# Optimization experiments

Hardware: AMD Instinct MI355X
Metric: run time of the kernel (lower is better)

Reference implementation:

```python
import jax, jax.numpy as jnp
import numpy as np

N_NODES = 100000


def gcn_conv(x, src, dst, W, b, n):
    # x: [N, F_in]; src/dst: [E+N] (self-loops already appended)
    h = x @ W  # [N, F_out]
    deg = jax.ops.segment_sum(jnp.ones_like(dst, dtype=h.dtype), dst, num_segments=n)
    dinv = jnp.where(deg > 0, jax.lax.rsqrt(deg), 0.0)
    norm = dinv[src] * dinv[dst]  # [E+N]
    msgs = h[src] * norm[:, None]  # gather + scale
    out = jax.ops.segment_sum(msgs, dst, num_segments=n)  # scatter-add at dst
    return out + b


def setup_inputs() -> dict:
    key = jax.random.key(0)
    k1, k2, k3, ke = jax.random.split(key, 4)
    d = 64
    x = jax.random.normal(k1, (N_NODES, d), dtype=jnp.float32)
    edge_index = jax.random.randint(ke, (2, 1000000), 0, N_NODES, dtype=jnp.int64)
    s = 1.0 / np.sqrt(d)
    W1 = jax.random.normal(k2, (d, d), dtype=jnp.float32) * s
    b1 = jnp.zeros((d,), dtype=jnp.float32)
    W2 = jax.random.normal(k3, (d, d), dtype=jnp.float32) * s
    b2 = jnp.zeros((d,), dtype=jnp.float32)
    return {"x": x, "edge_index": edge_index, "W1": W1, "b1": b1, "W2": W2, "b2": b2}


def reference(x, edge_index, W1, b1, W2, b2):
    n = x.shape[0]
    loops = jnp.arange(n, dtype=edge_index.dtype)
    src = jnp.concatenate([edge_index[0], loops])
    dst = jnp.concatenate([edge_index[1], loops])
    h = gcn_conv(x, src, dst, W1, b1, n)
    h = jax.nn.relu(h)
    out = gcn_conv(h, src, dst, W2, b2, n)
    return out
```

## Files before the change

kernel.cpp:

```cpp
#include <hip/hip_runtime.h>

#define F 64
#define NCH 256

typedef __attribute__((ext_vector_type(8))) short bf16x8;
typedef __attribute__((ext_vector_type(4))) float f32x4;

static __device__ __forceinline__ unsigned short f2bf(float f) {
    unsigned u = __float_as_uint(f);
    return (unsigned short)((u + 0x7fffu + ((u >> 16) & 1u)) >> 16);
}
static __device__ __forceinline__ float bflo(unsigned u) { return __uint_as_float(u << 16); }
static __device__ __forceinline__ float bfhi(unsigned u) { return __uint_as_float(u & 0xffff0000u); }

__global__ __launch_bounds__(256) void k_histprep(const int* __restrict__ dst,
                                                  int* __restrict__ histM,
                                                  const float* __restrict__ W1,
                                                  const float* __restrict__ W2,
                                                  unsigned short* __restrict__ W1t,
                                                  unsigned short* __restrict__ W2t,
                                                  int E, int chunk, int NB) {
    const int t = threadIdx.x;
    if (blockIdx.x >= NCH) {
        int which = blockIdx.x - NCH;
        const float* W = which ? W2 : W1;
        unsigned short* Wt = which ? W2t : W1t;
#pragma unroll
        for (int i = 0; i < 16; ++i) {
            int e = t + i * 256;
            int n = e >> 6, k = e & 63;
            Wt[e] = f2bf(W[k * 64 + n]);
        }
        return;
    }
    extern __shared__ int h[];
    for (int i = t; i < NB; i += 256) h[i] = 0;
    __syncthreads();
    const int lo = blockIdx.x * chunk;
    const int hi = min(E, lo + chunk);
    for (int e = lo + t; e < hi; e += 256) {
        atomicAdd(&h[dst[e] >> 8], 1);
    }
    __syncthreads();
    for (int i = t; i < NB; i += 256) histM[i * NCH + blockIdx.x] = h[i];
}

__global__ __launch_bounds__(256) void s_part(const int* __restrict__ v,
                                              int* __restrict__ part, int M) {
    __shared__ int sd[256];
    const int t = threadIdx.x;
    const int base = blockIdx.x * 1024 + t * 4;
    int s = 0;
    if (base + 3 < M) {
        int4 d = *(const int4*)&v[base];
        s = d.x + d.y + d.z + d.w;
    } else {
#pragma unroll
        for (int j = 0; j < 4; ++j) if (base + j < M) s += v[base + j];
    }
    sd[t] = s;
    __syncthreads();
    for (int off = 128; off > 0; off >>= 1) {
        if (t < off) sd[t] += sd[t + off];
        __syncthreads();
    }
    if (t == 0) part[blockIdx.x] = sd[0];
}

__global__ __launch_bounds__(256) void s_scanp(int* __restrict__ part, int nb) {
    __shared__ int sums[256];
    const int t = threadIdx.x;
    int s = (t < nb) ? part[t] : 0;
    sums[t] = s;
    __syncthreads();
    for (int off = 1; off < 256; off <<= 1) {
        int v = (t >= off) ? sums[t - off] : 0;
        __syncthreads();
        sums[t] += v;
        __syncthreads();
    }
    if (t < nb) part[t] = sums[t] - s;
}

__global__ __launch_bounds__(256) void s_emit(int* __restrict__ v,
                                              const int* __restrict__ part, int M) {
    __shared__ int sums[256];
    const int t = threadIdx.x;
    const int base = blockIdx.x * 1024 + t * 4;
    int d0 = 0, d1 = 0, d2 = 0, d3 = 0;
    if (base + 3 < M) {
        int4 d = *(const int4*)&v[base];
        d0 = d.x; d1 = d.y; d2 = d.z; d3 = d.w;
    } else {
        if (base + 0 < M) d0 = v[base + 0];
        if (base + 1 < M) d1 = v[base + 1];
        if (base + 2 < M) d2 = v[base + 2];
        if (base + 3 < M) d3 = v[base + 3];
    }
    int tot = d0 + d1 + d2 + d3;
    sums[t] = tot;
    __syncthreads();
    for (int off = 1; off < 256; off <<= 1) {
        int x = (t >= off) ? sums[t - off] : 0;
        __syncthreads();
        sums[t] += x;
        __syncthreads();
    }
    int o0 = part[blockIdx.x] + sums[t] - tot;
    int e0 = o0, e1 = o0 + d0, e2 = e1 + d1, e3 = e2 + d2;
    if (base + 3 < M) {
        *(int4*)&v[base] = make_int4(e0, e1, e2, e3);
    } else {
        int ee[4] = {e0, e1, e2, e3};
        for (int j = 0; j < 4; ++j) if (base + j < M) v[base + j] = ee[j];
    }
}

__global__ __launch_bounds__(256) void k_scatter2(const int* __restrict__ src,
                                                  const int* __restrict__ dst,
                                                  const int* __restrict__ scanM,
                                                  int* __restrict__ ebuf,
                                                  int E, int chunk, int NB) {
    extern __shared__ int cur[];
    const int t = threadIdx.x;
    for (int i = t; i < NB; i += 256) cur[i] = scanM[i * NCH + blockIdx.x];
    __syncthreads();
    const int lo = blockIdx.x * chunk;
    const int hi = min(E, lo + chunk);
    for (int e = lo + t; e < hi; e += 256) {
        int s = src[e];
        int d = dst[e];
        int p = atomicAdd(&cur[d >> 8], 1);
        ebuf[p] = s | ((d & 255) << 17);
    }
}

__global__ __launch_bounds__(256) void k_csr(const int* __restrict__ ebuf,
                                             const int* __restrict__ scanM,
                                             int* __restrict__ rowptr,
                                             int* __restrict__ csr,
                                             float* __restrict__ dinv,
                                             int N, int E, int NB) {
    __shared__ int hist[256];
    __shared__ int scn[256];
    __shared__ int cur[256];
    const int t = threadIdx.x;
    const int bkt = blockIdx.x;
    const int beg = scanM[bkt * NCH];
    const int end = (bkt + 1 < NB) ? scanM[(bkt + 1) * NCH] : E;

    hist[t] = 0;
    __syncthreads();
    for (int e = beg + t; e < end; e += 256)
        atomicAdd(&hist[((unsigned)ebuf[e]) >> 17], 1);
    __syncthreads();

    scn[t] = hist[t];
    __syncthreads();
    for (int off = 1; off < 256; off <<= 1) {
        int v = (t >= off) ? scn[t - off] : 0;
        __syncthreads();
        scn[t] += v;
        __syncthreads();
    }

    {
        int excl = scn[t] - hist[t];
        int rp = beg + excl;
        int node = (bkt << 8) + t;
        cur[t] = rp;
        if (node < N) {
            rowptr[node] = rp;
            dinv[node] = rsqrtf((float)(hist[t] + 1));
        }
    }
    if (bkt == NB - 1 && t == 0) rowptr[N] = E;
    __syncthreads();

    for (int e = beg + t; e < end; e += 256) {
        int pk = ebuf[e];
        int p = atomicAdd(&cur[((unsigned)pk) >> 17], 1);
        csr[p] = pk & 0x1FFFF;
    }
}

__global__ __launch_bounds__(256) void k_gemm1(const float* __restrict__ X,
                                               const unsigned short* __restrict__ W1t,
                                               const float* __restrict__ dinv,
                                               unsigned short* __restrict__ hs, int N) {
    __shared__ unsigned short Wl[64 * 72];
    __shared__ unsigned short Xs[64 * 72];
    const int t = threadIdx.x;
    const int row0 = blockIdx.x * 64;

#pragma unroll
    for (int i = 0; i < 2; ++i) {
        int idx = t + i * 256;
        int n = idx >> 3, k = (idx & 7) * 8;
        *(uint4*)&Wl[n * 72 + k] = ((const uint4*)W1t)[idx];
    }
#pragma unroll
    for (int i = 0; i < 4; ++i) {
        int idx = t + i * 256;
        int r = idx >> 4, c = (idx & 15) * 4;
        int gr = row0 + r;
        float4 v = make_float4(0.f, 0.f, 0.f, 0.f);
        if (gr < N) v = *(const float4*)&X[(size_t)gr * F + c];
        unsigned p0 = (unsigned)f2bf(v.x) | ((unsigned)f2bf(v.y) << 16);
        unsigned p1 = (unsigned)f2bf(v.z) | ((unsigned)f2bf(v.w) << 16);
        *(uint2*)&Xs[r * 72 + c] = make_uint2(p0, p1);
    }
    __syncthreads();

    const int w    = t >> 6;
    const int lane = t & 63;
    const int l15  = lane & 15;
    const int quad = lane >> 4;

    bf16x8 bf[4][2];
#pragma unroll
    for (int ct = 0; ct < 4; ++ct)
#pragma unroll
        for (int kc = 0; kc < 2; ++kc)
            bf[ct][kc] = *(const bf16x8*)&Wl[(ct * 16 + l15) * 72 + kc * 32 + quad * 8];

    const int am = w * 16 + l15;
    bf16x8 af0 = *(const bf16x8*)&Xs[am * 72 + quad * 8];
    bf16x8 af1 = *(const bf16x8*)&Xs[am * 72 + 32 + quad * 8];

    f32x4 acc[4];
#pragma unroll
    for (int ct = 0; ct < 4; ++ct) {
        f32x4 z = {0.f, 0.f, 0.f, 0.f};
        z = __builtin_amdgcn_mfma_f32_16x16x32_bf16(af0, bf[ct][0], z, 0, 0, 0);
        z = __builtin_amdgcn_mfma_f32_16x16x32_bf16(af1, bf[ct][1], z, 0, 0, 0);
        acc[ct] = z;
    }

    float dv[4];
#pragma unroll
    for (int r = 0; r < 4; ++r) {
        int row = row0 + w * 16 + quad * 4 + r;
        dv[r] = (row < N) ? dinv[row] : 0.f;
    }
#pragma unroll
    for (int ct = 0; ct < 4; ++ct) {
#pragma unroll
        for (int r = 0; r < 4; ++r) {
            int row = row0 + w * 16 + quad * 4 + r;
            if (row < N)
                hs[(size_t)row * F + ct * 16 + l15] = f2bf(acc[ct][r] * dv[r]);
        }
    }
}

__global__ __launch_bounds__(512) void k_aggmm(const unsigned short* __restrict__ hs1,
                                               const int* __restrict__ rowptr,
                                               const int* __restrict__ csr,
                                               const unsigned short* __restrict__ W2t,
                                               const float* __restrict__ b1,
                                               unsigned short* __restrict__ hs2, int N) {
    __shared__ unsigned short Act[256 * 72];
    __shared__ unsigned short Wl[64 * 72];
    __shared__ float sdv[256];
    const int t = threadIdx.x;
    const int node0 = blockIdx.x << 8;

    {
        int idx = t;
        int n = idx >> 3, k = (idx & 7) * 8;
        *(uint4*)&Wl[n * 72 + k] = ((const uint4*)W2t)[idx];
    }

    const int lane = t & 7;
    const int nsub = t >> 3;
    const uint4* hsb = (const uint4*)hs1;
    float4 bb0 = *(const float4*)&b1[lane * 8];
    float4 bb1 = *(const float4*)&b1[lane * 8 + 4];

#pragma unroll
    for (int it = 0; it < 4; ++it) {
        int local = it * 64 + nsub;
        int node = node0 + local;
        float sc = 0.f;
        unsigned p0 = 0, p1 = 0, p2 = 0, p3 = 0;
        if (node < N) {
            int beg = rowptr[node];
            int end = rowptr[node + 1];
            sc = rsqrtf((float)(end - beg + 1));
            float a0, a1, a2, a3, a4, a5, a6, a7;
            {
                uint4 u = hsb[(size_t)node * 8 + lane];
                a0 = bflo(u.x); a1 = bfhi(u.x);
                a2 = bflo(u.y); a3 = bfhi(u.y);
                a4 = bflo(u.z); a5 = bfhi(u.z);
                a6 = bflo(u.w); a7 = bfhi(u.w);
            }
            for (int base = beg; base < end; base += 16) {
                int i0 = base + lane;
                int i1 = base + 8 + lane;
                int x0 = (i0 < end) ? csr[i0] : 0;
                int x1 = (i1 < end) ? csr[i1] : 0;
                uint4 r[16];
#pragma unroll
                for (int k = 0; k < 8; ++k) {
                    int s = __shfl(x0, k, 8);
                    r[k] = hsb[(size_t)s * 8 + lane];
                }
#pragma unroll
                for (int k = 0; k < 8; ++k) {
                    int s = __shfl(x1, k, 8);
                    r[8 + k] = hsb[(size_t)s * 8 + lane];
                }
                int cnt = min(16, end - base);
#pragma unroll
                for (int k = 0; k < 16; ++k) {
                    if (k < cnt) {
                        uint4 u = r[k];
                        a0 += bflo(u.x); a1 += bfhi(u.x);
                        a2 += bflo(u.y); a3 += bfhi(u.y);
                        a4 += bflo(u.z); a5 += bfhi(u.z);
                        a6 += bflo(u.w); a7 += bfhi(u.w);
                    }
                }
            }
            float o0 = fmaxf(a0 * sc + bb0.x, 0.f), o1 = fmaxf(a1 * sc + bb0.y, 0.f);
            float o2 = fmaxf(a2 * sc + bb0.z, 0.f), o3 = fmaxf(a3 * sc + bb0.w, 0.f);
            float o4 = fmaxf(a4 * sc + bb1.x, 0.f), o5 = fmaxf(a5 * sc + bb1.y, 0.f);
            float o6 = fmaxf(a6 * sc + bb1.z, 0.f), o7 = fmaxf(a7 * sc + bb1.w, 0.f);
            p0 = (unsigned)f2bf(o0) | ((unsigned)f2bf(o1) << 16);
            p1 = (unsigned)f2bf(o2) | ((unsigned)f2bf(o3) << 16);
            p2 = (unsigned)f2bf(o4) | ((unsigned)f2bf(o5) << 16);
            p3 = (unsigned)f2bf(o6) | ((unsigned)f2bf(o7) << 16);
        }
        *(uint4*)&Act[local * 72 + lane * 8] = make_uint4(p0, p1, p2, p3);
        if (lane == 0) sdv[local] = sc;
    }
    __syncthreads();

    const int w    = t >> 6;
    const int l    = t & 63;
    const int l15  = l & 15;
    const int quad = l >> 4;

    bf16x8 bf[4][2];
#pragma unroll
    for (int nt = 0; nt < 4; ++nt)
#pragma unroll
        for (int kc = 0; kc < 2; ++kc)
            bf[nt][kc] = *(const bf16x8*)&Wl[(nt * 16 + l15) * 72 + kc * 32 + quad * 8];

#pragma unroll
    for (int mt = 0; mt < 2; ++mt) {
        int m0 = w * 32 + mt * 16;
        bf16x8 af0 = *(const bf16x8*)&Act[(m0 + l15) * 72 + quad * 8];
        bf16x8 af1 = *(const bf16x8*)&Act[(m0 + l15) * 72 + 32 + quad * 8];
#pragma unroll
        for (int nt = 0; nt < 4; ++nt) {
            f32x4 z = {0.f, 0.f, 0.f, 0.f};
            z = __builtin_amdgcn_mfma_f32_16x16x32_bf16(af0, bf[nt][0], z, 0, 0, 0);
            z = __builtin_amdgcn_mfma_f32_16x16x32_bf16(af1, bf[nt][1], z, 0, 0, 0);
#pragma unroll
            for (int r = 0; r < 4; ++r) {
                int row = m0 + quad * 4 + r;
                int node = node0 + row;
                if (node < N)
                    hs2[((size_t)nt * N + node) * 16 + l15] = f2bf(z[r] * sdv[row]);
            }
        }
    }
}

__global__ __launch_bounds__(256) void k_agg2(const unsigned short* __restrict__ hs2,
                                              const int* __restrict__ rowptr,
                                              const int* __restrict__ csr,
                                              const float* __restrict__ dinv,
                                              const float* __restrict__ b,
                                              float* __restrict__ out, int N) {
    const int slice = blockIdx.x & 3;
    const int chunk = blockIdx.x >> 2;
    const int t = threadIdx.x;
    const int node = chunk * 64 + (t >> 2);
    const int lane = t & 3;
    if (node >= N) return;
    const int beg = rowptr[node];
    const int end = rowptr[node + 1];
    const unsigned short* hp = hs2 + (size_t)slice * N * 16;

    float a[16];
#pragma unroll
    for (int j = 0; j < 16; ++j) a[j] = 0.f;

    int e = beg + lane;
    int i0 = (e < end) ? csr[e] : -1;
    int i1 = (e + 4 < end) ? csr[e + 4] : -1;
    while (i0 >= 0) {
        int i2 = (e + 8  < end) ? csr[e + 8]  : -1;
        int i3 = (e + 12 < end) ? csr[e + 12] : -1;
        {
            const uint4* p = (const uint4*)(hp + (size_t)i0 * 16);
            uint4 u0 = p[0];
            uint4 u1 = p[1];
            a[0] += bflo(u0.x); a[1] += bfhi(u0.x);
            a[2] += bflo(u0.y); a[3] += bfhi(u0.y);
            a[4] += bflo(u0.z); a[5] += bfhi(u0.z);
            a[6] += bflo(u0.w); a[7] += bfhi(u0.w);
            a[8]  += bflo(u1.x); a[9]  += bfhi(u1.x);
            a[10] += bflo(u1.y); a[11] += bfhi(u1.y);
            a[12] += bflo(u1.z); a[13] += bfhi(u1.z);
            a[14] += bflo(u1.w); a[15] += bfhi(u1.w);
        }
        if (i1 >= 0) {
            const uint4* p = (const uint4*)(hp + (size_t)i1 * 16);
            uint4 u0 = p[0];
            uint4 u1 = p[1];
            a[0] += bflo(u0.x); a[1] += bfhi(u0.x);
            a[2] += bflo(u0.y); a[3] += bfhi(u0.y);
            a[4] += bflo(u0.z); a[5] += bfhi(u0.z);
            a[6] += bflo(u0.w); a[7] += bfhi(u0.w);
            a[8]  += bflo(u1.x); a[9]  += bfhi(u1.x);
            a[10] += bflo(u1.y); a[11] += bfhi(u1.y);
            a[12] += bflo(u1.z); a[13] += bfhi(u1.z);
            a[14] += bflo(u1.w); a[15] += bfhi(u1.w);
        }
        i0 = i2;
        i1 = i3;
        e += 8;
    }

    float h[8];
#pragma unroll
    for (int k = 0; k < 8; ++k) {
        float lo = a[k]     + __shfl_xor(a[k], 2, 4);
        float hi = a[k + 8] + __shfl_xor(a[k + 8], 2, 4);
        h[k] = (lane & 2) ? hi : lo;
    }
    float v[4];
#pragma unroll
    for (int k = 0; k < 4; ++k) {
        float lo = h[k]     + __shfl_xor(h[k], 1, 4);
        float hi = h[k + 4] + __shfl_xor(h[k + 4], 1, 4);
        v[k] = (lane & 1) ? hi : lo;
    }

    const float sc = dinv[node];
    const int j0 = lane * 4;
    uint2 sv = *(const uint2*)(hp + (size_t)node * 16 + j0);
    float s0 = bflo(sv.x), s1 = bfhi(sv.x), s2 = bflo(sv.y), s3 = bfhi(sv.y);
    float4 bb = *(const float4*)&b[slice * 16 + j0];
    float4 o = make_float4((v[0] + s0) * sc + bb.x,
                           (v[1] + s1) * sc + bb.y,
                           (v[2] + s2) * sc + bb.z,
                           (v[3] + s3) * sc + bb.w);
    *(float4*)&out[(size_t)node * F + slice * 16 + j0] = o;
}

extern "C" void kernel_launch(void* const* d_in, const int* in_sizes, int n_in,
                              void* d_out, int out_size, void* d_ws, size_t ws_size,
                              hipStream_t stream) {
    const float* x  = (const float*)d_in[0];
    const int*   ei = (const int*)d_in[1];
    const float* W1 = (const float*)d_in[2];
    const float* b1 = (const float*)d_in[3];
    const float* W2 = (const float*)d_in[4];
    const float* b2 = (const float*)d_in[5];
    float* out = (float*)d_out;

    const int N = in_sizes[0] / F;
    const int E = in_sizes[1] / 2;
    const int* src = ei;
    const int* dst = ei + E;

    const int NB = (N + 255) >> 8;
    const int chunk = (E + NCH - 1) / NCH;
    const int M  = NB * NCH;
    const int Mp = ((M + 1023) / 1024) * 1024;
    const int nb2 = Mp / 1024;

    char* ws = (char*)d_ws;
    size_t a = 0;
    unsigned short* W1t = (unsigned short*)(ws + a); a += (4096 * 2 + 255) & ~(size_t)255;
    unsigned short* W2t = (unsigned short*)(ws + a); a += (4096 * 2 + 255) & ~(size_t)255;
    float* dinv   = (float*)(ws + a); a += ((size_t)N * 4 + 255) & ~(size_t)255;
    int*   part2  = (int*)(ws + a);   a += ((size_t)nb2 * 4 + 255) & ~(size_t)255;
    int*   rowptr = (int*)(ws + a);   a += ((size_t)(N + 1) * 4 + 255) & ~(size_t)255;
    int*   histM  = (int*)(ws + a);   a += ((size_t)Mp * 4 + 255) & ~(size_t)255;
    int*   ebuf   = (int*)(ws + a);   a += ((size_t)E * 4 + 255) & ~(size_t)255;
    int*   csr    = (int*)(ws + a);   a += ((size_t)E * 4 + 255) & ~(size_t)255;
    unsigned short* hs1 = (unsigned short*)(ws + a); a += ((size_t)N * F * 2 + 255) & ~(size_t)255;
    unsigned short* hs2 = (unsigned short*)(ws + a);

    const size_t ldsNB = (size_t)NB * 4;
    const int gGemm = (N + 63) / 64;
    const int gAgg2 = ((N + 63) / 64) * 4;

    k_histprep<<<NCH + 2, 256, ldsNB, stream>>>(dst, histM, W1, W2, W1t, W2t, E, chunk, NB);
    s_part<<<nb2, 256, 0, stream>>>(histM, part2, M);
    s_scanp<<<1, 256, 0, stream>>>(part2, nb2);
    s_emit<<<nb2, 256, 0, stream>>>(histM, part2, M);
    k_scatter2<<<NCH, 256, ldsNB, stream>>>(src, dst, histM, ebuf, E, chunk, NB);
    k_csr<<<NB, 256, 0, stream>>>(ebuf, histM, rowptr, csr, dinv, N, E, NB);

    k_gemm1<<<gGemm, 256, 0, stream>>>(x, W1t, dinv, hs1, N);
    k_aggmm<<<NB, 512, 0, stream>>>(hs1, rowptr, csr, W2t, b1, hs2, N);
    k_agg2<<<gAgg2, 256, 0, stream>>>(hs2, rowptr, csr, dinv, b2, out, N);
}
```

Measured before the change: 181.8 us.

## Fuse first GEMM into histogram kernel and apply source dinv during aggregation

The first-layer GEMM (X@W1) moves into the initial histogram/weight-prep kernel, so it no longer depends on dinv and runs concurrently with histogram blocks, removing one launch and the W1 transpose buffer. The source-side degree normalization is now applied inside the layer-1 aggregation by gathering dinv[src] per edge and using FMA. This adds an extra scattered 4-byte load per edge in the aggregation, and every GEMM block redoes the W1 transpose with strided global reads. The histogram LDS becomes a fixed 512-entry static array, which assumes NB <= 512.

```diff
diff --git a/kernel.cpp b/kernel.cpp
--- a/kernel.cpp
+++ b/kernel.cpp
@@ -13,36 +13,96 @@
 static __device__ __forceinline__ float bflo(unsigned u) { return __uint_as_float(u << 16); }
 static __device__ __forceinline__ float bfhi(unsigned u) { return __uint_as_float(u & 0xffff0000u); }
 
-__global__ __launch_bounds__(256) void k_histprep(const int* __restrict__ dst,
-                                                  int* __restrict__ histM,
-                                                  const float* __restrict__ W1,
-                                                  const float* __restrict__ W2,
-                                                  unsigned short* __restrict__ W1t,
-                                                  unsigned short* __restrict__ W2t,
-                                                  int E, int chunk, int NB) {
-    const int t = threadIdx.x;
-    if (blockIdx.x >= NCH) {
-        int which = blockIdx.x - NCH;
-        const float* W = which ? W2 : W1;
-        unsigned short* Wt = which ? W2t : W1t;
+__global__ __launch_bounds__(256) void k_fused0(const int* __restrict__ dst,
+                                                int* __restrict__ histM,
+                                                const float* __restrict__ W1,
+                                                const float* __restrict__ W2,
+                                                unsigned short* __restrict__ W2t,
+                                                const float* __restrict__ X,
+                                                unsigned short* __restrict__ hs1,
+                                                int E, int chunk, int NB, int N) {
+    __shared__ int h[512];
+    __shared__ unsigned short Wl[64 * 72];
+    __shared__ unsigned short Xs[64 * 72];
+    const int t = threadIdx.x;
+    const int b = blockIdx.x;
+
+    if (b < NCH) {
+        for (int i = t; i < NB; i += 256) h[i] = 0;
+        __syncthreads();
+        const int lo = b * chunk;
+        const int hi = min(E, lo + chunk);
+        for (int e = lo + t; e < hi; e += 256) {
+            atomicAdd(&h[dst[e] >> 8], 1);
+        }
+        __syncthreads();
+        for (int i = t; i < NB; i += 256) histM[i * NCH + b] = h[i];
+        return;
+    }
+    if (b == NCH) {
 #pragma unroll
         for (int i = 0; i < 16; ++i) {
             int e = t + i * 256;
             int n = e >> 6, k = e & 63;
-            Wt[e] = f2bf(W[k * 64 + n]);
+            W2t[e] = f2bf(W2[k * 64 + n]);
         }
         return;
     }
-    extern __shared__ int h[];
-    for (int i = t; i < NB; i += 256) h[i] = 0;
-    __syncthreads();
-    const int lo = blockIdx.x * chunk;
-    const int hi = min(E, lo + chunk);
-    for (int e = lo + t; e < hi; e += 256) {
-        atomicAdd(&h[dst[e] >> 8], 1);
-    }
-    __syncthreads();
-    for (int i = t; i < NB; i += 256) histM[i * NCH + blockIdx.x] = h[i];
+
+    const int row0 = (b - NCH - 1) * 64;
+#pragma unroll
+    for (int i = 0; i < 16; ++i) {
+        int e = t + i * 256;
+        int n = e >> 6, k = e & 63;
+        Wl[n * 72 + k] = f2bf(W1[k * 64 + n]);
+    }
+#pragma unroll
+    for (int i = 0; i < 4; ++i) {
+        int idx = t + i * 256;
+        int r = idx >> 4, c = (idx & 15) * 4;
+        int gr = row0 + r;
+        float4 v = make_float4(0.f, 0.f, 0.f, 0.f);
+        if (gr < N) v = *(const float4*)&X[(size_t)gr * F + c];
+        unsigned p0 = (unsigned)f2bf(v.x) | ((unsigned)f2bf(v.y) << 16);
+        unsigned p1 = (unsigned)f2bf(v.z) | ((unsigned)f2bf(v.w) << 16);
+        *(uint2*)&Xs[r * 72 + c] = make_uint2(p0, p1);
+    }
+    __syncthreads();
+
+    const int w    = t >> 6;
+    const int lane = t & 63;
+    const int l15  = lane & 15;
+    const int quad = lane >> 4;
+
+    bf16x8 bf[4][2];
+#pragma unroll
+    for (int ct = 0; ct < 4; ++ct)
+#pragma unroll
+        for (int kc = 0; kc < 2; ++kc)
+            bf[ct][kc] = *(const bf16x8*)&Wl[(ct * 16 + l15) * 72 + kc * 32 + quad * 8];
+
+    const int am = w * 16 + l15;
+    bf16x8 af0 = *(const bf16x8*)&Xs[am * 72 + quad * 8];
+    bf16x8 af1 = *(const bf16x8*)&Xs[am * 72 + 32 + quad * 8];
+
+    f32x4 acc[4];
+#pragma unroll
+    for (int ct = 0; ct < 4; ++ct) {
+        f32x4 z = {0.f, 0.f, 0.f, 0.f};
+        z = __builtin_amdgcn_mfma_f32_16x16x32_bf16(af0, bf[ct][0], z, 0, 0, 0);
+        z = __builtin_amdgcn_mfma_f32_16x16x32_bf16(af1, bf[ct][1], z, 0, 0, 0);
+        acc[ct] = z;
+    }
+
+#pragma unroll
+    for (int ct = 0; ct < 4; ++ct) {
+#pragma unroll
+        for (int r = 0; r < 4; ++r) {
+            int row = row0 + w * 16 + quad * 4 + r;
+            if (row < N)
+                hs1[(size_t)row * F + ct * 16 + l15] = f2bf(acc[ct][r]);
+        }
+    }
 }
 
 __global__ __launch_bounds__(256) void s_part(const int* __restrict__ v,
@@ -184,81 +244,12 @@
     }
 }
 
-__global__ __launch_bounds__(256) void k_gemm1(const float* __restrict__ X,
-                                               const unsigned short* __restrict__ W1t,
-                                               const float* __restrict__ dinv,
-                                               unsigned short* __restrict__ hs, int N) {
-    __shared__ unsigned short Wl[64 * 72];
-    __shared__ unsigned short Xs[64 * 72];
-    const int t = threadIdx.x;
-    const int row0 = blockIdx.x * 64;
-
-#pragma unroll
-    for (int i = 0; i < 2; ++i) {
-        int idx = t + i * 256;
-        int n = idx >> 3, k = (idx & 7) * 8;
-        *(uint4*)&Wl[n * 72 + k] = ((const uint4*)W1t)[idx];
-    }
-#pragma unroll
-    for (int i = 0; i < 4; ++i) {
-        int idx = t + i * 256;
-        int r = idx >> 4, c = (idx & 15) * 4;
-        int gr = row0 + r;
-        float4 v = make_float4(0.f, 0.f, 0.f, 0.f);
-        if (gr < N) v = *(const float4*)&X[(size_t)gr * F + c];
-        unsigned p0 = (unsigned)f2bf(v.x) | ((unsigned)f2bf(v.y) << 16);
-        unsigned p1 = (unsigned)f2bf(v.z) | ((unsigned)f2bf(v.w) << 16);
-        *(uint2*)&Xs[r * 72 + c] = make_uint2(p0, p1);
-    }
-    __syncthreads();
-
-    const int w    = t >> 6;
-    const int lane = t & 63;
-    const int l15  = lane & 15;
-    const int quad = lane >> 4;
-
-    bf16x8 bf[4][2];
-#pragma unroll
-    for (int ct = 0; ct < 4; ++ct)
-#pragma unroll
-        for (int kc = 0; kc < 2; ++kc)
-            bf[ct][kc] = *(const bf16x8*)&Wl[(ct * 16 + l15) * 72 + kc * 32 + quad * 8];
-
-    const int am = w * 16 + l15;
-    bf16x8 af0 = *(const bf16x8*)&Xs[am * 72 + quad * 8];
-    bf16x8 af1 = *(const bf16x8*)&Xs[am * 72 + 32 + quad * 8];
-
-    f32x4 acc[4];
-#pragma unroll
-    for (int ct = 0; ct < 4; ++ct) {
-        f32x4 z = {0.f, 0.f, 0.f, 0.f};
-        z = __builtin_amdgcn_mfma_f32_16x16x32_bf16(af0, bf[ct][0], z, 0, 0, 0);
-        z = __builtin_amdgcn_mfma_f32_16x16x32_bf16(af1, bf[ct][1], z, 0, 0, 0);
-        acc[ct] = z;
-    }
-
-    float dv[4];
-#pragma unroll
-    for (int r = 0; r < 4; ++r) {
-        int row = row0 + w * 16 + quad * 4 + r;
-        dv[r] = (row < N) ? dinv[row] : 0.f;
-    }
-#pragma unroll
-    for (int ct = 0; ct < 4; ++ct) {
-#pragma unroll
-        for (int r = 0; r < 4; ++r) {
-            int row = row0 + w * 16 + quad * 4 + r;
-            if (row < N)
-                hs[(size_t)row * F + ct * 16 + l15] = f2bf(acc[ct][r] * dv[r]);
-        }
-    }
-}
-
 __global__ __launch_bounds__(512) void k_aggmm(const unsigned short* __restrict__ hs1,
                                                const int* __restrict__ rowptr,
                                                const int* __restrict__ csr,
                                                const unsigned short* __restrict__ W2t,
                                                const float* __restrict__ b1,
+                                               const float* __restrict__ dinv,
                                                unsigned short* __restrict__ hs2, int N) {
     __shared__ unsigned short Act[256 * 72];
     __shared__ unsigned short Wl[64 * 72];
@@ -291,10 +282,10 @@
             float a0, a1, a2, a3, a4, a5, a6, a7;
             {
                 uint4 u = hsb[(size_t)node * 8 + lane];
-                a0 = bflo(u.x); a1 = bfhi(u.x);
-                a2 = bflo(u.y); a3 = bfhi(u.y);
-                a4 = bflo(u.z); a5 = bfhi(u.z);
-                a6 = bflo(u.w); a7 = bfhi(u.w);
+                a0 = sc * bflo(u.x); a1 = sc * bfhi(u.x);
+                a2 = sc * bflo(u.y); a3 = sc * bfhi(u.y);
+                a4 = sc * bflo(u.z); a5 = sc * bfhi(u.z);
+                a6 = sc * bflo(u.w); a7 = sc * bfhi(u.w);
             }
             for (int base = beg; base < end; base += 16) {
                 int i0 = base + lane;
@@ -302,25 +293,29 @@
                 int x0 = (i0 < end) ? csr[i0] : 0;
                 int x1 = (i1 < end) ? csr[i1] : 0;
                 uint4 r[16];
+                float dv[16];
 #pragma unroll
                 for (int k = 0; k < 8; ++k) {
                     int s = __shfl(x0, k, 8);
                     r[k] = hsb[(size_t)s * 8 + lane];
+                    dv[k] = dinv[s];
                 }
 #pragma unroll
                 for (int k = 0; k < 8; ++k) {
                     int s = __shfl(x1, k, 8);
                     r[8 + k] = hsb[(size_t)s * 8 + lane];
+                    dv[8 + k] = dinv[s];
                 }
                 int cnt = min(16, end - base);
 #pragma unroll
                 for (int k = 0; k < 16; ++k) {
                     if (k < cnt) {
                         uint4 u = r[k];
-                        a0 += bflo(u.x); a1 += bfhi(u.x);
-                        a2 += bflo(u.y); a3 += bfhi(u.y);
-                        a4 += bflo(u.z); a5 += bfhi(u.z);
-                        a6 += bflo(u.w); a7 += bfhi(u.w);
+                        float w = dv[k];
+                        a0 = fmaf(bflo(u.x), w, a0); a1 = fmaf(bfhi(u.x), w, a1);
+                        a2 = fmaf(bflo(u.y), w, a2); a3 = fmaf(bfhi(u.y), w, a3);
+                        a4 = fmaf(bflo(u.z), w, a4); a5 = fmaf(bfhi(u.z), w, a5);
+                        a6 = fmaf(bflo(u.w), w, a6); a7 = fmaf(bfhi(u.w), w, a7);
                     }
                 }
             }
@@ -479,7 +474,6 @@
 
     char* ws = (char*)d_ws;
     size_t a = 0;
-    unsigned short* W1t = (unsigned short*)(ws + a); a += (4096 * 2 + 255) & ~(size_t)255;
     unsigned short* W2t = (unsigned short*)(ws + a); a += (4096 * 2 + 255) & ~(size_t)255;
     float* dinv   = (float*)(ws + a); a += ((size_t)N * 4 + 255) & ~(size_t)255;
     int*   part2  = (int*)(ws + a);   a += ((size_t)nb2 * 4 + 255) & ~(size_t)255;
@@ -494,14 +488,14 @@
     const int gGemm = (N + 63) / 64;
     const int gAgg2 = ((N + 63) / 64) * 4;
 
-    k_histprep<<<NCH + 2, 256, ldsNB, stream>>>(dst, histM, W1, W2, W1t, W2t, E, chunk, NB);
+    k_fused0<<<NCH + 1 + gGemm, 256, 0, stream>>>(dst, histM, W1, W2, W2t, x, hs1,
+                                                  E, chunk, NB, N);
     s_part<<<nb2, 256, 0, stream>>>(histM, part2, M);
     s_scanp<<<1, 256, 0, stream>>>(part2, nb2);
     s_emit<<<nb2, 256, 0, stream>>>(histM, part2, M);
     k_scatter2<<<NCH, 256, ldsNB, stream>>>(src, dst, histM, ebuf, E, chunk, NB);
     k_csr<<<NB, 256, 0, stream>>>(ebuf, histM, rowptr, csr, dinv, N, E, NB);
 
-    k_gemm1<<<gGemm, 256, 0, stream>>>(x, W1t, dinv, hs1, N);
-    k_aggmm<<<NB, 512, 0, stream>>>(hs1, rowptr, csr, W2t, b1, hs2, N);
+    k_aggmm<<<NB, 512, 0, stream>>>(hs1, rowptr, csr, W2t, b1, dinv, hs2, N);
     k_agg2<<<gAgg2, 256, 0, stream>>>(hs2, rowptr, csr, dinv, b2, out, N);
 }
```

Result: slower. 193.4 us (+6.4%).

## Merge preprocessing kernels and overlap scatter with first GEMM via global degree atomics

Applied to the files above, without the earlier changes.

The degree count moves out of k_csr into a separate global-atomic pass, so dinv is available before the CSR build. That lets the first GEMM run in the same launch as the edge scatter. The scan's middle kernel is removed by having each emit block reduce the partial sums itself, and zeroing, scan partials and degree counting are folded into existing launches. This cuts the launch count from nine to seven and overlaps independent work. In exchange it adds a million global atomics on deg and a fixed 512-entry LDS histogram that assumes NB is at most 512.

```diff
diff --git a/kernel.cpp b/kernel.cpp
--- a/kernel.cpp
+++ b/kernel.cpp
@@ -13,16 +13,28 @@
 static __device__ __forceinline__ float bflo(unsigned u) { return __uint_as_float(u << 16); }
 static __device__ __forceinline__ float bfhi(unsigned u) { return __uint_as_float(u & 0xffff0000u); }
 
-__global__ __launch_bounds__(256) void k_histprep(const int* __restrict__ dst,
-                                                  int* __restrict__ histM,
-                                                  const float* __restrict__ W1,
-                                                  const float* __restrict__ W2,
-                                                  unsigned short* __restrict__ W1t,
-                                                  unsigned short* __restrict__ W2t,
-                                                  int E, int chunk, int NB) {
-    const int t = threadIdx.x;
-    if (blockIdx.x >= NCH) {
-        int which = blockIdx.x - NCH;
+__global__ __launch_bounds__(256) void k_fused0(const int* __restrict__ dst,
+                                                int* __restrict__ histM,
+                                                const float* __restrict__ W1,
+                                                const float* __restrict__ W2,
+                                                unsigned short* __restrict__ W1t,
+                                                unsigned short* __restrict__ W2t,
+                                                int* __restrict__ deg,
+                                                int E, int chunk, int NB, int N) {
+    __shared__ int h[512];
+    const int t = threadIdx.x;
+    const int b = blockIdx.x;
+    if (b >= NCH + 2) {
+        int base = (b - NCH - 2) * 1024 + t * 4;
+        if (base + 3 < N) {
+            *(int4*)&deg[base] = make_int4(0, 0, 0, 0);
+        } else {
+            for (int j = 0; j < 4; ++j) if (base + j < N) deg[base + j] = 0;
+        }
+        return;
+    }
+    if (b >= NCH) {
+        int which = b - NCH;
         const float* W = which ? W2 : W1;
         unsigned short* Wt = which ? W2t : W1t;
 #pragma unroll
@@ -33,23 +45,34 @@
         }
         return;
     }
-    extern __shared__ int h[];
     for (int i = t; i < NB; i += 256) h[i] = 0;
     __syncthreads();
-    const int lo = blockIdx.x * chunk;
+    const int lo = b * chunk;
     const int hi = min(E, lo + chunk);
     for (int e = lo + t; e < hi; e += 256) {
         atomicAdd(&h[dst[e] >> 8], 1);
     }
     __syncthreads();
-    for (int i = t; i < NB; i += 256) histM[i * NCH + blockIdx.x] = h[i];
-}
-
-__global__ __launch_bounds__(256) void s_part(const int* __restrict__ v,
-                                              int* __restrict__ part, int M) {
+    for (int i = t; i < NB; i += 256) histM[i * NCH + b] = h[i];
+}
+
+__global__ __launch_bounds__(256) void k_partdeg(const int* __restrict__ v,
+                                                 int* __restrict__ part,
+                                                 const int* __restrict__ dst,
+                                                 int* __restrict__ deg,
+                                                 int M, int E, int chunk, int nb) {
     __shared__ int sd[256];
     const int t = threadIdx.x;
-    const int base = blockIdx.x * 1024 + t * 4;
+    const int b = blockIdx.x;
+    if (b >= nb) {
+        const int c = b - nb;
+        const int lo = c * chunk;
+        const int hi = min(E, lo + chunk);
+        for (int e = lo + t; e < hi; e += 256)
+            atomicAdd(&deg[dst[e]], 1);
+        return;
+    }
+    const int base = b * 1024 + t * 4;
     int s = 0;
     if (base + 3 < M) {
         int4 d = *(const int4*)&v[base];
@@ -64,29 +87,40 @@
         if (t < off) sd[t] += sd[t + off];
         __syncthreads();
     }
-    if (t == 0) part[blockIdx.x] = sd[0];
-}
-
-__global__ __launch_bounds__(256) void s_scanp(int* __restrict__ part, int nb) {
+    if (t == 0) part[b] = sd[0];
+}
+
+__global__ __launch_bounds__(256) void k_emitdinv(int* __restrict__ v,
+                                                  const int* __restrict__ part,
+                                                  const int* __restrict__ deg,
+                                                  float* __restrict__ dinv,
+                                                  int M, int N, int nb) {
     __shared__ int sums[256];
-    const int t = threadIdx.x;
-    int s = (t < nb) ? part[t] : 0;
-    sums[t] = s;
-    __syncthreads();
-    for (int off = 1; off < 256; off <<= 1) {
-        int v = (t >= off) ? sums[t - off] : 0;
-        __syncthreads();
-        sums[t] += v;
-        __syncthreads();
-    }
-    if (t < nb) part[t] = sums[t] - s;
-}
-
-__global__ __launch_bounds__(256) void s_emit(int* __restrict__ v,
-                                              const int* __restrict__ part, int M) {
-    __shared__ int sums[256];
-    const int t = threadIdx.x;
-    const int base = blockIdx.x * 1024 + t * 4;
+    __shared__ int red[256];
+    const int t = threadIdx.x;
+    const int b = blockIdx.x;
+    if (b >= nb) {
+        int base = (b - nb) * 1024 + t * 4;
+        if (base + 3 < N) {
+            int4 d = *(const int4*)&deg[base];
+            float4 o = make_float4(rsqrtf((float)(d.x + 1)), rsqrtf((float)(d.y + 1)),
+                                   rsqrtf((float)(d.z + 1)), rsqrtf((float)(d.w + 1)));
+            *(float4*)&dinv[base] = o;
+        } else {
+            for (int j = 0; j < 4; ++j)
+                if (base + j < N) dinv[base + j] = rsqrtf((float)(deg[base + j] + 1));
+        }
+        return;
+    }
+    red[t] = (t < b) ? part[t] : 0;
+    __syncthreads();
+    for (int off = 128; off > 0; off >>= 1) {
+        if (t < off) red[t] += red[t + off];
+        __syncthreads();
+    }
+    const int pref = red[0];
+
+    const int base = b * 1024 + t * 4;
     int d0 = 0, d1 = 0, d2 = 0, d3 = 0;
     if (base + 3 < M) {
         int4 d = *(const int4*)&v[base];
@@ -106,7 +140,7 @@
         sums[t] += x;
         __syncthreads();
     }
-    int o0 = part[blockIdx.x] + sums[t] - tot;
+    int o0 = pref + sums[t] - tot;
     int e0 = o0, e1 = o0 + d0, e2 = e1 + d1, e3 = e2 + d2;
     if (base + 3 < M) {
         *(int4*)&v[base] = make_int4(e0, e1, e2, e3);
@@ -116,83 +150,38 @@
     }
 }
 
-__global__ __launch_bounds__(256) void k_scatter2(const int* __restrict__ src,
+__global__ __launch_bounds__(256) void k_scatgemm(const int* __restrict__ src,
                                                   const int* __restrict__ dst,
                                                   const int* __restrict__ scanM,
                                                   int* __restrict__ ebuf,
-                                                  int E, int chunk, int NB) {
-    extern __shared__ int cur[];
-    const int t = threadIdx.x;
-    for (int i = t; i < NB; i += 256) cur[i] = scanM[i * NCH + blockIdx.x];
-    __syncthreads();
-    const int lo = blockIdx.x * chunk;
-    const int hi = min(E, lo + chunk);
-    for (int e = lo + t; e < hi; e += 256) {
-        int s = src[e];
-        int d = dst[e];
-        int p = atomicAdd(&cur[d >> 8], 1);
-        ebuf[p] = s | ((d & 255) << 17);
-    }
-}
-
-__global__ __launch_bounds__(256) void k_csr(const int* __restrict__ ebuf,
-                                             const int* __restrict__ scanM,
-                                             int* __restrict__ rowptr,
-                                             int* __restrict__ csr,
-                                             float* __restrict__ dinv,
-                                             int N, int E, int NB) {
-    __shared__ int hist[256];
-    __shared__ int scn[256];
-    __shared__ int cur[256];
-    const int t = threadIdx.x;
-    const int bkt = blockIdx.x;
-    const int beg = scanM[bkt * NCH];
-    const int end = (bkt + 1 < NB) ? scanM[(bkt + 1) * NCH] : E;
-
-    hist[t] = 0;
-    __syncthreads();
-    for (int e = beg + t; e < end; e += 256)
-        atomicAdd(&hist[((unsigned)ebuf[e]) >> 17], 1);
-    __syncthreads();
-
-    scn[t] = hist[t];
-    __syncthreads();
-    for (int off = 1; off < 256; off <<= 1) {
-        int v = (t >= off) ? scn[t - off] : 0;
-        __syncthreads();
-        scn[t] += v;
-        __syncthreads();
-    }
-
-    {
-        int excl = scn[t] - hist[t];
-        int rp = beg + excl;
-        int node = (bkt << 8) + t;
-        cur[t] = rp;
-        if (node < N) {
-            rowptr[node] = rp;
-            dinv[node] = rsqrtf((float)(hist[t] + 1));
-        }
-    }
-    if (bkt == NB - 1 && t == 0) rowptr[N] = E;
-    __syncthreads();
-
-    for (int e = beg + t; e < end; e += 256) {
-        int pk = ebuf[e];
-        int p = atomicAdd(&cur[((unsigned)pk) >> 17], 1);
-        csr[p] = pk & 0x1FFFF;
-    }
-}
-
-__global__ __launch_bounds__(256) void k_gemm1(const float* __restrict__ X,
-                                               const unsigned short* __restrict__ W1t,
-                                               const float* __restrict__ dinv,
-                                               unsigned short* __restrict__ hs, int N) {
-    __shared__ unsigned short Wl[64 * 72];
-    __shared__ unsigned short Xs[64 * 72];
-    const int t = threadIdx.x;
-    const int row0 = blockIdx.x * 64;
-
+                                                  const float* __restrict__ X,
+                                                  const unsigned short* __restrict__ W1t,
+                                                  const float* __restrict__ dinv,
+                                                  unsigned short* __restrict__ hs1,
+                                                  int E, int chunk, int NB, int N) {
+    __shared__ unsigned short SMa[64 * 72];
+    __shared__ unsigned short SMb[64 * 72];
+    const int t = threadIdx.x;
+    const int b = blockIdx.x;
+
+    if (b < NCH) {
+        int* cur = (int*)SMa;
+        for (int i = t; i < NB; i += 256) cur[i] = scanM[i * NCH + b];
+        __syncthreads();
+        const int lo = b * chunk;
+        const int hi = min(E, lo + chunk);
+        for (int e = lo + t; e < hi; e += 256) {
+            int s = src[e];
+            int d = dst[e];
+            int p = atomicAdd(&cur[d >> 8], 1);
+            ebuf[p] = s | ((d & 255) << 17);
+        }
+        return;
+    }
+
+    unsigned short* Wl = SMa;
+    unsigned short* Xs = SMb;
+    const int row0 = (b - NCH) * 64;
 #pragma unroll
     for (int i = 0; i < 2; ++i) {
         int idx = t + i * 256;
@@ -249,8 +238,53 @@
         for (int r = 0; r < 4; ++r) {
             int row = row0 + w * 16 + quad * 4 + r;
             if (row < N)
-                hs[(size_t)row * F + ct * 16 + l15] = f2bf(acc[ct][r] * dv[r]);
-        }
+                hs1[(size_t)row * F + ct * 16 + l15] = f2bf(acc[ct][r] * dv[r]);
+        }
+    }
+}
+
+__global__ __launch_bounds__(256) void k_csr(const int* __restrict__ ebuf,
+                                             const int* __restrict__ scanM,
+                                             int* __restrict__ rowptr,
+                                             int* __restrict__ csr,
+                                             int N, int E, int NB) {
+    __shared__ int hist[256];
+    __shared__ int scn[256];
+    __shared__ int cur[256];
+    const int t = threadIdx.x;
+    const int bkt = blockIdx.x;
+    const int beg = scanM[bkt * NCH];
+    const int end = (bkt + 1 < NB) ? scanM[(bkt + 1) * NCH] : E;
+
+    hist[t] = 0;
+    __syncthreads();
+    for (int e = beg + t; e < end; e += 256)
+        atomicAdd(&hist[((unsigned)ebuf[e]) >> 17], 1);
+    __syncthreads();
+
+    scn[t] = hist[t];
+    __syncthreads();
+    for (int off = 1; off < 256; off <<= 1) {
+        int v = (t >= off) ? scn[t - off] : 0;
+        __syncthreads();
+        scn[t] += v;
+        __syncthreads();
+    }
+
+    {
+        int excl = scn[t] - hist[t];
+        int rp = beg + excl;
+        int node = (bkt << 8) + t;
+        cur[t] = rp;
+        if (node < N) rowptr[node] = rp;
+    }
+    if (bkt == NB - 1 && t == 0) rowptr[N] = E;
+    __syncthreads();
+
+    for (int e = beg + t; e < end; e += 256) {
+        int pk = ebuf[e];
+        int p = atomicAdd(&cur[((unsigned)pk) >> 17], 1);
+        csr[p] = pk & 0x1FFFF;
     }
 }
 
@@ -481,6 +515,7 @@
     size_t a = 0;
     unsigned short* W1t = (unsigned short*)(ws + a); a += (4096 * 2 + 255) & ~(size_t)255;
     unsigned short* W2t = (unsigned short*)(ws + a); a += (4096 * 2 + 255) & ~(size_t)255;
+    int*   deg    = (int*)(ws + a);   a += ((size_t)N * 4 + 255) & ~(size_t)255;
     float* dinv   = (float*)(ws + a); a += ((size_t)N * 4 + 255) & ~(size_t)255;
     int*   part2  = (int*)(ws + a);   a += ((size_t)nb2 * 4 + 255) & ~(size_t)255;
     int*   rowptr = (int*)(ws + a);   a += ((size_t)(N + 1) * 4 + 255) & ~(size_t)255;
@@ -490,18 +525,17 @@
     unsigned short* hs1 = (unsigned short*)(ws + a); a += ((size_t)N * F * 2 + 255) & ~(size_t)255;
     unsigned short* hs2 = (unsigned short*)(ws + a);
 
-    const size_t ldsNB = (size_t)NB * 4;
+    const int gZ    = (N + 1023) / 1024;
     const int gGemm = (N + 63) / 64;
     const int gAgg2 = ((N + 63) / 64) * 4;
 
-    k_histprep<<<NCH + 2, 256, ldsNB, stream>>>(dst, histM, W1, W2, W1t, W2t, E, chunk, NB);
-    s_part<<<nb2, 256, 0, stream>>>(histM, part2, M);
-    s_scanp<<<1, 256, 0, stream>>>(part2, nb2);
-    s_emit<<<nb2, 256, 0, stream>>>(histM, part2, M);
-    k_scatter2<<<NCH, 256, ldsNB, stream>>>(src, dst, histM, ebuf, E, chunk, NB);
-    k_csr<<<NB, 256, 0, stream>>>(ebuf, histM, rowptr, csr, dinv, N, E, NB);
-
-    k_gemm1<<<gGemm, 256, 0, stream>>>(x, W1t, dinv, hs1, N);
+    k_fused0<<<NCH + 2 + gZ, 256, 0, stream>>>(dst, histM, W1, W2, W1t, W2t, deg,
+                                               E, chunk, NB, N);
+    k_partdeg<<<nb2 + NCH, 256, 0, stream>>>(histM, part2, dst, deg, M, E, chunk, nb2);
+    k_emitdinv<<<nb2 + gZ, 256, 0, stream>>>(histM, part2, deg, dinv, M, N, nb2);
+    k_scatgemm<<<NCH + gGemm, 256, 0, stream>>>(src, dst, histM, ebuf, x, W1t, dinv,
+                                                hs1, E, chunk, NB, N);
+    k_csr<<<NB, 256, 0, stream>>>(ebuf, histM, rowptr, csr, N, E, NB);
     k_aggmm<<<NB, 512, 0, stream>>>(hs1, rowptr, csr, W2t, b1, hs2, N);
     k_agg2<<<gAgg2, 256, 0, stream>>>(hs2, rowptr, csr, dinv, b2, out, N);
 }
```

After: 220.5 us. 1.21x slower.
